# Performance work log

Measured on AMD Instinct MI355X. Metric: run time of the kernel, lower is better.

The kernel has to match this reference:

```python
import jax, jax.numpy as jnp
import numpy as np

B, S, D, H, HD = 1, 4096, 768, 12, 64
L, C, WIN, NCLS = 2, 256, 256, 64
NC = S // C
V, FF = 50265, 3072
NEG = -1e9
SCALE = np.float32(1.0 / np.sqrt(HD))


def setup_inputs() -> dict:
    key = jax.random.key(0)
    ks = jax.random.split(key, 32)
    p = lambda k, shape: (0.02 * jax.random.normal(k, shape)).astype(jnp.float32)
    inp = {
        'x': jax.random.randint(ks[0], (B, S), 0, V, dtype=jnp.int32),
        'mask_src': jnp.ones((B, S), dtype=jnp.int32),
        'clss': jnp.sort(jax.random.randint(ks[1], (B, NCLS), 0, S, dtype=jnp.int32), axis=-1),
        'segs': jax.random.randint(ks[2], (B, S), 0, 2, dtype=jnp.int32),
        'word_emb': p(ks[3], (V, D)),
        'pos_emb': p(ks[4], (S, D)),
        'type_emb': p(ks[5], (2, D)),
        'ln_e_s': jnp.ones((D,), jnp.float32), 'ln_e_b': jnp.zeros((D,), jnp.float32),
        'Wq': p(ks[6], (L, D, D)), 'bq': jnp.zeros((L, D), jnp.float32),
        'Wk': p(ks[7], (L, D, D)), 'bk': jnp.zeros((L, D), jnp.float32),
        'Wv': p(ks[8], (L, D, D)), 'bv': jnp.zeros((L, D), jnp.float32),
        'Wqg': p(ks[9], (L, D, D)), 'bqg': jnp.zeros((L, D), jnp.float32),
        'Wkg': p(ks[10], (L, D, D)), 'bkg': jnp.zeros((L, D), jnp.float32),
        'Wvg': p(ks[11], (L, D, D)), 'bvg': jnp.zeros((L, D), jnp.float32),
        'Wo': p(ks[12], (L, D, D)), 'bo': jnp.zeros((L, D), jnp.float32),
        'ln1_s': jnp.ones((L, D), jnp.float32), 'ln1_b': jnp.zeros((L, D), jnp.float32),
        'Wf1': p(ks[13], (L, D, FF)), 'bf1': jnp.zeros((L, FF), jnp.float32),
        'Wf2': p(ks[14], (L, FF, D)), 'bf2': jnp.zeros((L, D), jnp.float32),
        'ln2_s': jnp.ones((L, D), jnp.float32), 'ln2_b': jnp.zeros((L, D), jnp.float32),
    }
    return inp


def _layer_norm(x, s, b):
    m = jnp.mean(x, -1, keepdims=True)
    v = jnp.mean((x - m) ** 2, -1, keepdims=True)
    return (x - m) * jax.lax.rsqrt(v + 1e-5) * s + b


def _forward(x, mask_src, clss, segs, word_emb, pos_emb, type_emb, ln_e_s, ln_e_b,
             Wq, bq, Wk, bk, Wv, bv, Wqg, bqg, Wkg, bkg, Wvg, bvg, Wo, bo,
             ln1_s, ln1_b, Wf1, bf1, Wf2, bf2, ln2_s, ln2_b):
    # global positions: union of all clss values, same for every batch row
    g_idx = clss.reshape(-1)                                       # [NCLS]
    is_glb = jnp.zeros((S,), bool).at[g_idx].set(True)             # [S]
    kvalid = (mask_src > 0) & (~is_glb)[None, :]                   # band keys: no pad, no global
    gi = (jnp.arange(NC) * C)[:, None] + jnp.arange(3 * C)[None, :]  # gather idx into padded seq
    rel = jnp.arange(3 * C)[None, :] - (jnp.arange(C)[:, None] + C)  # key offset from query
    band_ok = jnp.abs(rel) <= WIN                                   # [C,3C]
    kv3 = jnp.pad(kvalid, ((0, 0), (C, C)))[:, gi]                  # [B,NC,3C]
    bmask = band_ok[None, None, None, :, :] & kv3[:, None, :, None, :]  # [B,1,NC,C,3C]
    gkey_ok = (mask_src[:, g_idx] > 0)[:, None, None, :]            # [B,1,1,NCLS]
    full_ok = (mask_src > 0)[:, None, None, :]                      # [B,1,1,S]

    h = _layer_norm(word_emb[x] + pos_emb[jnp.arange(S)][None] + type_emb[segs], ln_e_s, ln_e_b)

    for l in range(L):
        q = ((h @ Wq[l] + bq[l]).reshape(B, S, H, HD)) * SCALE
        k = (h @ Wk[l] + bk[l]).reshape(B, S, H, HD)
        v = (h @ Wv[l] + bv[l]).reshape(B, S, H, HD)
        # --- sliding-window band attention ---
        k3 = jnp.pad(k, ((0, 0), (C, C), (0, 0), (0, 0)))[:, gi]    # [B,NC,3C,H,HD]
        v3 = jnp.pad(v, ((0, 0), (C, C), (0, 0), (0, 0)))[:, gi]
        qc = q.reshape(B, NC, C, H, HD)
        sb = jnp.einsum('bnqhd,bnkhd->bhnqk', qc, k3)               # [B,H,NC,C,3C]
        sb = jnp.where(bmask, sb, NEG)
        # --- global keys seen by every query ---
        kg, vg = k[:, g_idx], v[:, g_idx]                           # [B,NCLS,H,HD]
        sg = jnp.einsum('bshd,bkhd->bhsk', q, kg)                   # [B,H,S,NCLS]
        sg = jnp.where(gkey_ok, sg, NEG)
        scores = jnp.concatenate([sg, sb.reshape(B, H, S, 3 * C)], -1)
        probs = jax.nn.softmax(scores, axis=-1)
        pg = probs[..., :NCLS]
        pb = probs[..., NCLS:].reshape(B, H, NC, C, 3 * C)
        out = jnp.einsum('bhnqk,bnkhd->bnqhd', pb, v3).reshape(B, S, H, HD)
        out = out + jnp.einsum('bhsk,bkhd->bshd', pg, vg)
        # --- global query tokens: full attention with *_global projections ---
        hg = h[:, g_idx]                                            # [B,NCLS,D]
        qg = ((hg @ Wqg[l] + bqg[l]).reshape(B, NCLS, H, HD)) * SCALE
        kgf = (h @ Wkg[l] + bkg[l]).reshape(B, S, H, HD)
        vgf = (h @ Wvg[l] + bvg[l]).reshape(B, S, H, HD)
        sfull = jnp.einsum('bqhd,bkhd->bhqk', qg, kgf)              # [B,H,NCLS,S]
        sfull = jnp.where(full_ok, sfull, NEG)
        og = jnp.einsum('bhqk,bkhd->bqhd', jax.nn.softmax(sfull, -1), vgf)
        out = out.at[:, g_idx].set(og)
        # --- output proj, residual, LN, FFN ---
        attn_out = out.reshape(B, S, D) @ Wo[l] + bo[l]
        h = _layer_norm(h + attn_out, ln1_s[l], ln1_b[l])
        ff = jax.nn.gelu(h @ Wf1[l] + bf1[l]) @ Wf2[l] + bf2[l]
        h = _layer_norm(h + ff, ln2_s[l], ln2_b[l])
    return h


def reference(x, mask_src, clss, segs, word_emb, pos_emb, type_emb, ln_e_s, ln_e_b,
              Wq, bq, Wk, bk, Wv, bv, Wqg, bqg, Wkg, bkg, Wvg, bvg, Wo, bo,
              ln1_s, ln1_b, Wf1, bf1, Wf2, bf2, ln2_s, ln2_b):
    return _forward(x, mask_src, clss, segs, word_emb, pos_emb, type_emb, ln_e_s, ln_e_b,
                    Wq, bq, Wk, bk, Wv, bv, Wqg, bqg, Wkg, bkg, Wvg, bvg, Wo, bo,
                    ln1_s, ln1_b, Wf1, bf1, Wf2, bf2, ln2_s, ln2_b)
```

## Files before the change

kernel.cpp:

```cpp
#include <hip/hip_runtime.h>
#include <hip/hip_bf16.h>
#include <cstdint>

#define SEQ  4096
#define DIM  768
#define NH   12
#define HDIM 64
#define NLAYER 2
#define CHK  256
#define WINR 256
#define NCLS 64
#define NCHK 16
#define FFD  3072
#define QSCALE 0.125f
#define LOG2E 1.44269504f
#define QSC2 (QSCALE * LOG2E)
#define SD ((size_t)SEQ * DIM)
#define PS_LD 72
#define TK 32

typedef __attribute__((__vector_size__(16))) float floatx4;
typedef __attribute__((ext_vector_type(8))) __bf16 bf16x8;

__device__ __forceinline__ void async16(const void* g, void* l) {
    __builtin_amdgcn_global_load_lds(
        (const __attribute__((address_space(1))) uint32_t*)g,
        (__attribute__((address_space(3))) uint32_t*)l, 16, 0, 0);
}

__device__ __forceinline__ float block_reduce_sum(float v, float* red) {
    int t = threadIdx.x;
    red[t] = v; __syncthreads();
    #pragma unroll
    for (int st = 128; st > 0; st >>= 1) {
        if (t < st) red[t] += red[t + st];
        __syncthreads();
    }
    float r = red[0]; __syncthreads();
    return r;
}

__device__ __forceinline__ float gelu_f(float x) {
    float x3 = x * x * x;
    return 0.5f * x * (1.0f + tanhf(0.7978845608028654f * (x + 0.044715f * x3)));
}

__global__ __launch_bounds__(256) void setup_kernel(
    const float* __restrict__ bq, const float* __restrict__ bk, const float* __restrict__ bv,
    const float* __restrict__ bkg, const float* __restrict__ bvg,
    float* __restrict__ bqkv, int* __restrict__ isglb, int* __restrict__ glb_rank)
{
    int idx = blockIdx.x * 256 + threadIdx.x;
    int l = idx / 3840, c = idx % 3840, j = c / 768, d = c % 768;
    const float* s = (j == 0) ? bq : (j == 1) ? bk : (j == 2) ? bv : (j == 3) ? bkg : bvg;
    bqkv[idx] = s[l * 768 + d];
    if (idx < SEQ) { isglb[idx] = 0; glb_rank[idx] = -1; }
}
__global__ __launch_bounds__(64) void set_rank_kernel(
    const int* __restrict__ clss, int* __restrict__ isglb, int* __restrict__ glb_rank)
{
    int t = threadIdx.x;
    int p = clss[t];
    isglb[p] = 1;
    glb_rank[p] = t;
}

__global__ __launch_bounds__(256) void embed_ln_kernel(
    const int* __restrict__ x, const int* __restrict__ segs,
    const float* __restrict__ word_emb, const float* __restrict__ pos_emb,
    const float* __restrict__ type_emb, const float* __restrict__ gs,
    const float* __restrict__ gb, float* __restrict__ h, __bf16* __restrict__ hb)
{
    __shared__ float red[256];
    int s = blockIdx.x, t = threadIdx.x;
    int w = x[s], sg = segs[s];
    float v0[3]; float lsum = 0.f;
    #pragma unroll
    for (int i = 0; i < 3; i++) {
        int d = t + i * 256;
        float val = word_emb[(size_t)w * DIM + d] + pos_emb[(size_t)s * DIM + d]
                  + type_emb[(size_t)sg * DIM + d];
        v0[i] = val; lsum += val;
    }
    float mean = block_reduce_sum(lsum, red) * (1.0f / DIM);
    float lv = 0.f;
    #pragma unroll
    for (int i = 0; i < 3; i++) { float dv = v0[i] - mean; lv += dv * dv; }
    float var = block_reduce_sum(lv, red) * (1.0f / DIM);
    float rstd = rsqrtf(var + 1e-5f);
    #pragma unroll
    for (int i = 0; i < 3; i++) {
        int d = t + i * 256;
        float o = (v0[i] - mean) * rstd * gs[d] + gb[d];
        h[(size_t)s * DIM + d] = o;
        hb[(size_t)s * DIM + d] = (__bf16)o;
    }
}

__global__ __launch_bounds__(256) void add_ln_kernel(
    float* __restrict__ h, const float* __restrict__ r,
    const float* __restrict__ gs, const float* __restrict__ gb,
    __bf16* __restrict__ hb)
{
    __shared__ float red[256];
    int s = blockIdx.x, t = threadIdx.x;
    float v0[3]; float lsum = 0.f;
    #pragma unroll
    for (int i = 0; i < 3; i++) {
        int d = t + i * 256;
        float val = h[(size_t)s * DIM + d] + r[(size_t)s * DIM + d];
        v0[i] = val; lsum += val;
    }
    float mean = block_reduce_sum(lsum, red) * (1.0f / DIM);
    float lv = 0.f;
    #pragma unroll
    for (int i = 0; i < 3; i++) { float dv = v0[i] - mean; lv += dv * dv; }
    float var = block_reduce_sum(lv, red) * (1.0f / DIM);
    float rstd = rsqrtf(var + 1e-5f);
    #pragma unroll
    for (int i = 0; i < 3; i++) {
        int d = t + i * 256;
        float o = (v0[i] - mean) * rstd * gs[d] + gb[d];
        h[(size_t)s * DIM + d] = o;
        hb[(size_t)s * DIM + d] = (__bf16)o;
    }
}

struct Ptr16 { const float* p[16]; };
__global__ __launch_bounds__(256) void transpose_w_kernel(
    Ptr16 in, __bf16* __restrict__ out, int K, int N)
{
    __shared__ float tile[32][33];
    const float* src = in.p[blockIdx.z];
    __bf16* dst = out + (size_t)blockIdx.z * K * N;
    int bx = blockIdx.x * 32;
    int by = blockIdx.y * 32;
    int tx = threadIdx.x & 31, ty = threadIdx.x >> 5;
    #pragma unroll
    for (int i = 0; i < 32; i += 8)
        tile[ty + i][tx] = src[(size_t)(by + ty + i) * N + bx + tx];
    __syncthreads();
    #pragma unroll
    for (int i = 0; i < 32; i += 8)
        dst[(size_t)(bx + ty + i) * K + by + tx] = (__bf16)tile[tx][ty + i];
}

template<int TMv, int TNv>
__global__ __launch_bounds__(256) void mfma_gemm_t(
    const __bf16* __restrict__ A, const __bf16* __restrict__ Bt,
    const float* __restrict__ bias, float* __restrict__ Cf,
    __bf16* __restrict__ Cb, int M, int N, int K, float scale, int act)
{
    constexpr int AM = TMv / 32, AN = TNv / 32;
    constexpr int CA = TMv / 64, CB = TNv / 64;
    __shared__ __align__(16) __bf16 As[TMv * TK];
    __shared__ __align__(16) __bf16 Bs[TNv * TK];
    int t = threadIdx.x;
    int wave = t >> 6, lane = t & 63;
    int bm = blockIdx.x * TMv, bn = blockIdx.y * TNv;
    int wm = (wave & 1) * (TMv / 2), wn = (wave >> 1) * (TNv / 2);

    floatx4 acc[AM][AN];
    #pragma unroll
    for (int i = 0; i < AM; i++)
        #pragma unroll
        for (int j = 0; j < AN; j++) { floatx4 z = {0.f,0.f,0.f,0.f}; acc[i][j] = z; }

    const int mrow = lane & 15, kq = (lane >> 4) * 8;

    for (int k0 = 0; k0 < K; k0 += TK) {
        __syncthreads();
        #pragma unroll
        for (int i = 0; i < CA; i++) {
            int c = i * 256 + wave * 64 + lane;
            async16(A + (size_t)(bm + (c >> 2)) * K + k0 + (c & 3) * 8,
                    &As[(size_t)(i * 256 + wave * 64) * 8]);
        }
        #pragma unroll
        for (int i = 0; i < CB; i++) {
            int c = i * 256 + wave * 64 + lane;
            async16(Bt + (size_t)(bn + (c >> 2)) * K + k0 + (c & 3) * 8,
                    &Bs[(size_t)(i * 256 + wave * 64) * 8]);
        }
        __builtin_amdgcn_s_waitcnt(0x0f70);
        __syncthreads();
        bf16x8 af[AM], bfr[AN];
        #pragma unroll
        for (int mt = 0; mt < AM; mt++)
            af[mt] = *(const bf16x8*)&As[(wm + mt * 16 + mrow) * TK + kq];
        #pragma unroll
        for (int nt = 0; nt < AN; nt++)
            bfr[nt] = *(const bf16x8*)&Bs[(wn + nt * 16 + mrow) * TK + kq];
        #pragma unroll
        for (int mt = 0; mt < AM; mt++)
            #pragma unroll
            for (int nt = 0; nt < AN; nt++)
                acc[mt][nt] = __builtin_amdgcn_mfma_f32_16x16x32_bf16(
                    af[mt], bfr[nt], acc[mt][nt], 0, 0, 0);
    }

    int col_l = lane & 15, row_l = (lane >> 4) * 4;
    #pragma unroll
    for (int nt = 0; nt < AN; nt++) {
        int col = bn + wn + nt * 16 + col_l;
        float bs = bias[col];
        #pragma unroll
        for (int mt = 0; mt < AM; mt++) {
            floatx4 v = acc[mt][nt];
            int row0 = bm + wm + mt * 16 + row_l;
            #pragma unroll
            for (int rr = 0; rr < 4; rr++) {
                float o = (v[rr] + bs) * scale;
                if (act) o = gelu_f(o);
                if (Cf) Cf[(size_t)(row0 + rr) * N + col] = o;
                if (Cb) Cb[(size_t)(row0 + rr) * N + col] = (__bf16)o;
            }
        }
    }
}

__global__ __launch_bounds__(256) void mfma_gemm_proj(
    const __bf16* __restrict__ A, const __bf16* __restrict__ Bt,
    const float* __restrict__ bias,
    __bf16* __restrict__ qb, __bf16* __restrict__ kb,
    __bf16* __restrict__ vb, __bf16* __restrict__ vtg,
    __bf16* __restrict__ kgb, __bf16* __restrict__ vgt, int K)
{
    __shared__ __align__(16) __bf16 As[128 * TK];
    __shared__ __align__(16) __bf16 Bs[128 * TK];
    int t = threadIdx.x;
    int wave = t >> 6, lane = t & 63;
    int bm = blockIdx.x * 128, bn = blockIdx.y * 128;
    int wm = (wave & 1) * 64, wn = (wave >> 1) * 64;

    floatx4 acc[4][4];
    #pragma unroll
    for (int i = 0; i < 4; i++)
        #pragma unroll
        for (int j = 0; j < 4; j++) { floatx4 z = {0.f,0.f,0.f,0.f}; acc[i][j] = z; }

    const int mrow = lane & 15, kq = (lane >> 4) * 8;

    for (int k0 = 0; k0 < K; k0 += TK) {
        __syncthreads();
        #pragma unroll
        for (int i = 0; i < 2; i++) {
            int c = i * 256 + wave * 64 + lane;
            async16(A + (size_t)(bm + (c >> 2)) * K + k0 + (c & 3) * 8,
                    &As[(size_t)(i * 256 + wave * 64) * 8]);
            async16(Bt + (size_t)(bn + (c >> 2)) * K + k0 + (c & 3) * 8,
                    &Bs[(size_t)(i * 256 + wave * 64) * 8]);
        }
        __builtin_amdgcn_s_waitcnt(0x0f70);
        __syncthreads();
        bf16x8 af[4], bfr[4];
        #pragma unroll
        for (int mt = 0; mt < 4; mt++)
            af[mt] = *(const bf16x8*)&As[(wm + mt * 16 + mrow) * TK + kq];
        #pragma unroll
        for (int nt = 0; nt < 4; nt++)
            bfr[nt] = *(const bf16x8*)&Bs[(wn + nt * 16 + mrow) * TK + kq];
        #pragma unroll
        for (int mt = 0; mt < 4; mt++)
            #pragma unroll
            for (int nt = 0; nt < 4; nt++)
                acc[mt][nt] = __builtin_amdgcn_mfma_f32_16x16x32_bf16(
                    af[mt], bfr[nt], acc[mt][nt], 0, 0, 0);
    }

    int col_l = lane & 15, row_l = (lane >> 4) * 4;
    int seg = bn / 768;
    int colw_base = bn - seg * 768 + wn;
    float scl = (seg == 0) ? QSC2 : 1.0f;
    #pragma unroll
    for (int nt = 0; nt < 4; nt++) {
        int col = bn + wn + nt * 16 + col_l;
        int colw = colw_base + nt * 16 + col_l;
        float bs = bias[col];
        #pragma unroll
        for (int mt = 0; mt < 4; mt++) {
            floatx4 v = acc[mt][nt];
            int row0 = bm + wm + mt * 16 + row_l;
            __bf16 t4[4];
            #pragma unroll
            for (int rr = 0; rr < 4; rr++) t4[rr] = (__bf16)((v[rr] + bs) * scl);
            if (seg <= 2 || seg == 3) {
                __bf16* dst = (seg == 0) ? qb : (seg == 1) ? kb : (seg == 2) ? vb : kgb;
                #pragma unroll
                for (int rr = 0; rr < 4; rr++)
                    dst[(size_t)(row0 + rr) * 768 + colw] = t4[rr];
            }
            if (seg == 2)
                *(uint2*)&vtg[(size_t)colw * SEQ + row0] = *(uint2*)t4;
            if (seg == 4)
                *(uint2*)&vgt[(size_t)colw * SEQ + row0] = *(uint2*)t4;
        }
    }
}

__global__ __launch_bounds__(256) void qg_proj(
    const __bf16* __restrict__ hb, const __bf16* __restrict__ Bt,
    const int* __restrict__ clss, const float* __restrict__ bias,
    __bf16* __restrict__ out)
{
    __shared__ __align__(16) __bf16 As[64 * TK];
    __shared__ __align__(16) __bf16 Bs[128 * TK];
    int t = threadIdx.x;
    int wave = t >> 6, lane = t & 63;
    int bn = blockIdx.y * 128;
    int wm = (wave & 1) * 32, wn = (wave >> 1) * 64;

    int cA = wave * 64 + lane;
    int grow = clss[cA >> 2];

    floatx4 acc[2][4];
    #pragma unroll
    for (int i = 0; i < 2; i++)
        #pragma unroll
        for (int j = 0; j < 4; j++) { floatx4 z = {0.f,0.f,0.f,0.f}; acc[i][j] = z; }

    const int mrow = lane & 15, kq = (lane >> 4) * 8;

    for (int k0 = 0; k0 < DIM; k0 += TK) {
        __syncthreads();
        async16(hb + (size_t)grow * DIM + k0 + (cA & 3) * 8,
                &As[(size_t)(wave * 64) * 8]);
        #pragma unroll
        for (int i = 0; i < 2; i++) {
            int c = i * 256 + wave * 64 + lane;
            async16(Bt + (size_t)(bn + (c >> 2)) * DIM + k0 + (c & 3) * 8,
                    &Bs[(size_t)(i * 256 + wave * 64) * 8]);
        }
        __builtin_amdgcn_s_waitcnt(0x0f70);
        __syncthreads();
        bf16x8 af[2], bfr[4];
        #pragma unroll
        for (int mt = 0; mt < 2; mt++)
            af[mt] = *(const bf16x8*)&As[(wm + mt * 16 + mrow) * TK + kq];
        #pragma unroll
        for (int nt = 0; nt < 4; nt++)
            bfr[nt] = *(const bf16x8*)&Bs[(wn + nt * 16 + mrow) * TK + kq];
        #pragma unroll
        for (int mt = 0; mt < 2; mt++)
            #pragma unroll
            for (int nt = 0; nt < 4; nt++)
                acc[mt][nt] = __builtin_amdgcn_mfma_f32_16x16x32_bf16(
                    af[mt], bfr[nt], acc[mt][nt], 0, 0, 0);
    }
    int col_l = lane & 15, row_l = (lane >> 4) * 4;
    #pragma unroll
    for (int nt = 0; nt < 4; nt++) {
        int col = bn + wn + nt * 16 + col_l;
        float bs = bias[col];
        #pragma unroll
        for (int mt = 0; mt < 2; mt++) {
            floatx4 v = acc[mt][nt];
            int row0 = wm + mt * 16 + row_l;
            #pragma unroll
            for (int rr = 0; rr < 4; rr++)
                out[(size_t)(row0 + rr) * DIM + col] = (__bf16)((v[rr] + bs) * QSC2);
        }
    }
}

__global__ __launch_bounds__(256) void attn_kernel(
    const __bf16* __restrict__ qb, const __bf16* __restrict__ kb,
    const __bf16* __restrict__ vb, const __bf16* __restrict__ vtg,
    const __bf16* __restrict__ qgbb, const __bf16* __restrict__ kgb,
    const __bf16* __restrict__ vgt,
    const int* __restrict__ clss, const int* __restrict__ mask_src,
    const int* __restrict__ is_glb,
    float* __restrict__ OpartB, float* __restrict__ mlpartB,
    float* __restrict__ OpartG, float* __restrict__ mlpartG)
{
    __shared__ __align__(16) __bf16 Kt[4096];
    __shared__ __align__(16) __bf16 Vt[4096];
    __shared__ __align__(16) __bf16 Ps[4][32 * PS_LD];
    __shared__ int kvalid[64];
    __shared__ int gpos[64];

    const int hh = blockIdx.y;
    const int t = threadIdx.x, wave = t >> 6, lane = t & 63;
    const int quad = lane >> 4, col_l = lane & 15, row_l = quad * 4;
    const int l3 = lane & 3, l2h = lane >> 2, l7 = lane & 7, l3h = lane >> 3;
    __bf16* PsW = Ps[wave];

    if (blockIdx.z >= 4) {
        const int sp = blockIdx.x * 2 + (blockIdx.z - 4);
        bf16x8 aq[2];
        {
            const __bf16* qp = qgbb + (size_t)(wave * 16 + col_l) * DIM + hh * HDIM;
            aq[0] = *(const bf16x8*)(qp + quad * 8);
            aq[1] = *(const bf16x8*)(qp + 32 + quad * 8);
        }
        floatx4 oacc[4];
        #pragma unroll
        for (int i = 0; i < 4; i++) { floatx4 z = {0.f,0.f,0.f,0.f}; oacc[i] = z; }
        float m4[4], l4[4];
        #pragma unroll
        for (int r = 0; r < 4; r++) { m4[r] = -1e30f; l4[r] = 0.f; }

        for (int tt = 0; tt < 2; tt++) {
            int pos0 = sp * 128 + tt * 64;
            __syncthreads();
            if (t < 64) kvalid[t] = (mask_src[pos0 + t] > 0) ? 1 : 0;
            #pragma unroll
            for (int ii = 0; ii < 2; ii++) {
                int gid = wave * 2 + ii;
                int p = gid >> 2, kbase = (gid & 3) * 16;
                async16(kgb + (size_t)(pos0 + kbase + l2h) * DIM + hh * HDIM + p * 32 + l3 * 8,
                        &Kt[p * 2048 + kbase * 32]);
            }
            #pragma unroll
            for (int ii = 0; ii < 2; ii++) {
                int gid = wave * 2 + ii;
                int p = gid >> 2, dbase = (gid & 3) * 16;
                async16(vgt + (size_t)(hh * HDIM + dbase + l2h) * SEQ + pos0 + p * 32 + l3 * 8,
                        &Vt[p * 2048 + dbase * 32]);
            }
            __builtin_amdgcn_s_waitcnt(0x0f70);
            __syncthreads();

            floatx4 s[4];
            #pragma unroll
            for (int nt = 0; nt < 4; nt++) {
                bf16x8 b0 = *(const bf16x8*)&Kt[(nt * 16 + col_l) * 32 + quad * 8];
                bf16x8 b1 = *(const bf16x8*)&Kt[2048 + (nt * 16 + col_l) * 32 + quad * 8];
                floatx4 z = {0.f,0.f,0.f,0.f};
                z = __builtin_amdgcn_mfma_f32_16x16x32_bf16(aq[0], b0, z, 0,0,0);
                z = __builtin_amdgcn_mfma_f32_16x16x32_bf16(aq[1], b1, z, 0,0,0);
                s[nt] = z;
            }
            #pragma unroll
            for (int nt = 0; nt < 4; nt++) {
                int kvv = kvalid[nt * 16 + col_l];
                #pragma unroll
                for (int rr = 0; rr < 4; rr++)
                    if (!kvv) s[nt][rr] = -1e30f;
            }
            #pragma unroll
            for (int rr = 0; rr < 4; rr++) {
                float rm = fmaxf(fmaxf(s[0][rr], s[1][rr]), fmaxf(s[2][rr], s[3][rr]));
                rm = fmaxf(rm, __shfl_xor(rm, 1));
                rm = fmaxf(rm, __shfl_xor(rm, 2));
                rm = fmaxf(rm, __shfl_xor(rm, 4));
                rm = fmaxf(rm, __shfl_xor(rm, 8));
                float mo = m4[rr];
                float mn = fmaxf(mo, rm);
                float alpha = exp2f(mo - mn);
                float rsum = 0.f;
                #pragma unroll
                for (int nt = 0; nt < 4; nt++) {
                    float p = exp2f(s[nt][rr] - mn);
                    rsum += p;
                    PsW[(row_l + rr) * PS_LD + nt * 16 + col_l] = (__bf16)p;
                }
                rsum += __shfl_xor(rsum, 1);
                rsum += __shfl_xor(rsum, 2);
                rsum += __shfl_xor(rsum, 4);
                rsum += __shfl_xor(rsum, 8);
                l4[rr] = l4[rr] * alpha + rsum;
                m4[rr] = mn;
                #pragma unroll
                for (int nt = 0; nt < 4; nt++) oacc[nt][rr] *= alpha;
            }
            bf16x8 ap0 = *(const bf16x8*)&PsW[col_l * PS_LD + quad * 8];
            bf16x8 ap1 = *(const bf16x8*)&PsW[col_l * PS_LD + 32 + quad * 8];
            #pragma unroll
            for (int nt = 0; nt < 4; nt++) {
                bf16x8 b0 = *(const bf16x8*)&Vt[(nt * 16 + col_l) * 32 + quad * 8];
                bf16x8 b1 = *(const bf16x8*)&Vt[2048 + (nt * 16 + col_l) * 32 + quad * 8];
                oacc[nt] = __builtin_amdgcn_mfma_f32_16x16x32_bf16(ap0, b0, oacc[nt], 0,0,0);
                oacc[nt] = __builtin_amdgcn_mfma_f32_16x16x32_bf16(ap1, b1, oacc[nt], 0,0,0);
            }
        }
        size_t base = (size_t)(hh * 32 + sp) * 64;
        #pragma unroll
        for (int nt = 0; nt < 4; nt++)
            #pragma unroll
            for (int rr = 0; rr < 4; rr++)
                OpartG[(base + wave * 16 + row_l + rr) * 64 + nt * 16 + col_l] = oacc[nt][rr];
        if (col_l == 0) {
            #pragma unroll
            for (int rr = 0; rr < 4; rr++) {
                mlpartG[(base + wave * 16 + row_l + rr) * 2]     = m4[rr];
                mlpartG[(base + wave * 16 + row_l + rr) * 2 + 1] = l4[rr];
            }
        }
        return;
    }

    const int n = blockIdx.x, zi = blockIdx.z;
    const int qh = zi >> 1, ks = zi & 1;
    const int qw = qh * 128 + wave * 32;

    if (t < 64) gpos[t] = clss[t];

    bf16x8 aq[2][2];
    #pragma unroll
    for (int mt = 0; mt < 2; mt++) {
// ... 118 lines not shown
                float mo = mrw[ri];
                float mn = fmaxf(mo, rm);
                float alpha = exp2f(mo - mn);
                float rsum = 0.f;
                #pragma unroll
                for (int nt = 0; nt < 4; nt++) {
                    float p = exp2f(s[nt][rr] - mn);
                    rsum += p;
                    PsW[(mt * 16 + row_l + rr) * PS_LD + nt * 16 + col_l] = (__bf16)p;
                }
                rsum += __shfl_xor(rsum, 1);
                rsum += __shfl_xor(rsum, 2);
                rsum += __shfl_xor(rsum, 4);
                rsum += __shfl_xor(rsum, 8);
                lrw[ri] = lrw[ri] * alpha + rsum;
                mrw[ri] = mn;
                #pragma unroll
                for (int nt = 0; nt < 4; nt++) oacc[mt][nt][rr] *= alpha;
            }
        }
        bf16x8 bvf[4][2], ap[2][2];
        #pragma unroll
        for (int nt = 0; nt < 4; nt++) {
            bvf[nt][0] = *(const bf16x8*)&Vt[(nt * 16 + col_l) * 32 + quad * 8];
            bvf[nt][1] = *(const bf16x8*)&Vt[2048 + (nt * 16 + col_l) * 32 + quad * 8];
        }
        #pragma unroll
        for (int mt = 0; mt < 2; mt++) {
            ap[mt][0] = *(const bf16x8*)&PsW[(mt * 16 + col_l) * PS_LD + quad * 8];
            ap[mt][1] = *(const bf16x8*)&PsW[(mt * 16 + col_l) * PS_LD + 32 + quad * 8];
        }
        #pragma unroll
        for (int mt = 0; mt < 2; mt++)
            #pragma unroll
            for (int nt = 0; nt < 4; nt++) {
                oacc[mt][nt] = __builtin_amdgcn_mfma_f32_16x16x32_bf16(
                    ap[mt][0], bvf[nt][0], oacc[mt][nt], 0,0,0);
                oacc[mt][nt] = __builtin_amdgcn_mfma_f32_16x16x32_bf16(
                    ap[mt][1], bvf[nt][1], oacc[mt][nt], 0,0,0);
            }
    }

    #pragma unroll
    for (int mt = 0; mt < 2; mt++) {
        #pragma unroll
        for (int rr = 0; rr < 4; rr++) {
            int srow = n * CHK + qw + mt * 16 + row_l + rr;
            size_t rbase = ((size_t)ks * SEQ + srow) * NH + hh;
            #pragma unroll
            for (int nt = 0; nt < 4; nt++)
                OpartB[rbase * 64 + nt * 16 + col_l] = oacc[mt][nt][rr];
            if (col_l == 0) {
                mlpartB[rbase * 2]     = mrw[mt * 4 + rr];
                mlpartB[rbase * 2 + 1] = lrw[mt * 4 + rr];
            }
        }
    }
}

__global__ __launch_bounds__(256) void attn_finalize(
    const float* __restrict__ OpartB, const float* __restrict__ mlpartB,
    const float* __restrict__ OpartG, const float* __restrict__ mlpartG,
    const int* __restrict__ glb_rank, __bf16* __restrict__ outb)
{
    int g = threadIdx.x >> 6, d = threadIdx.x & 63;
    int s = blockIdx.x * 4 + g, hh = blockIdx.y;
    int r = glb_rank[s];
    float o;
    if (r >= 0) {
        float M = -1e30f;
        for (int sp = 0; sp < 32; sp++)
            M = fmaxf(M, mlpartG[(((size_t)hh * 32 + sp) * 64 + r) * 2]);
        float L = 0.f, acc = 0.f;
        for (int sp = 0; sp < 32; sp++) {
            size_t b = ((size_t)hh * 32 + sp) * 64 + r;
            float w = exp2f(mlpartG[b * 2] - M);
            L += mlpartG[b * 2 + 1] * w;
            acc += w * OpartG[b * 64 + d];
        }
        o = acc / L;
    } else {
        size_t r0 = ((size_t)s) * NH + hh;
        size_t r1 = ((size_t)SEQ + s) * NH + hh;
        float m0 = mlpartB[r0 * 2], l0 = mlpartB[r0 * 2 + 1];
        float m1 = mlpartB[r1 * 2], l1 = mlpartB[r1 * 2 + 1];
        float M = fmaxf(m0, m1);
        float w0 = exp2f(m0 - M), w1 = exp2f(m1 - M);
        o = (OpartB[r0 * 64 + d] * w0 + OpartB[r1 * 64 + d] * w1) / (l0 * w0 + l1 * w1);
    }
    outb[(size_t)s * DIM + hh * HDIM + d] = (__bf16)o;
}

extern "C" void kernel_launch(void* const* d_in, const int* in_sizes, int n_in,
                              void* d_out, int out_size, void* d_ws, size_t ws_size,
                              hipStream_t stream)
{
    const int* x        = (const int*)d_in[0];
    const int* mask_src = (const int*)d_in[1];
    const int* clss     = (const int*)d_in[2];
    const int* segs     = (const int*)d_in[3];
    const float* word_emb = (const float*)d_in[4];
    const float* pos_emb  = (const float*)d_in[5];
    const float* type_emb = (const float*)d_in[6];
    const float* ln_e_s   = (const float*)d_in[7];
    const float* ln_e_b   = (const float*)d_in[8];
    const float* Wq  = (const float*)d_in[9];
    const float* bq  = (const float*)d_in[10];
    const float* Wk  = (const float*)d_in[11];
    const float* bk  = (const float*)d_in[12];
    const float* Wv  = (const float*)d_in[13];
    const float* bv  = (const float*)d_in[14];
    const float* Wqg = (const float*)d_in[15];
    const float* bqg = (const float*)d_in[16];
    const float* Wkg = (const float*)d_in[17];
    const float* bkg = (const float*)d_in[18];
    const float* Wvg = (const float*)d_in[19];
    const float* bvg = (const float*)d_in[20];
    const float* Wo  = (const float*)d_in[21];
    const float* bo  = (const float*)d_in[22];
    const float* ln1_s = (const float*)d_in[23];
    const float* ln1_b = (const float*)d_in[24];
    const float* Wf1 = (const float*)d_in[25];
    const float* bf1 = (const float*)d_in[26];
    const float* Wf2 = (const float*)d_in[27];
    const float* bf2 = (const float*)d_in[28];
    const float* ln2_s = (const float*)d_in[29];
    const float* ln2_b = (const float*)d_in[30];

    const size_t DD = (size_t)DIM * DIM;
    float* ws = (float*)d_ws;
    float*  h    = ws;
    float*  s4   = ws + SD;
    __bf16* hb   = (__bf16*)(ws + 2 * SD);
    __bf16* b6b  = (__bf16*)(ws + 2 * SD) + SD;
    __bf16* qb   = (__bf16*)(ws + 3 * SD);
    __bf16* kb   = (__bf16*)(ws + 3 * SD) + SD;
    __bf16* vb   = (__bf16*)(ws + 4 * SD);
    __bf16* vtg  = (__bf16*)(ws + 4 * SD) + SD;
    __bf16* kgb  = (__bf16*)(ws + 5 * SD);
    __bf16* vgt  = (__bf16*)(ws + 5 * SD) + SD;
    __bf16* gelu_b = qb;
    float* extra = ws + 6 * SD;
    __bf16* Wbf   = (__bf16*)extra;
    float* after_w = extra + 15 * DD;
    float* bqkv   = after_w;
    float* OpartG = bqkv + 7680;
    float* mlpartG= OpartG + 1572864;
    float* OpartB = mlpartG + 49152;
    float* mlpartB= OpartB + 6291456;
    __bf16* qgbb  = (__bf16*)(mlpartB + 196608);
    int*   isglb  = (int*)(qgbb + (size_t)NCLS * DIM);
    int*   grank  = isglb + SEQ;

    setup_kernel<<<30, 256, 0, stream>>>(bq, bk, bv, bkg, bvg, bqkv, isglb, grank);
    set_rank_kernel<<<1, 64, 0, stream>>>(clss, isglb, grank);
    embed_ln_kernel<<<SEQ, 256, 0, stream>>>(x, segs, word_emb, pos_emb, type_emb,
                                             ln_e_s, ln_e_b, h, hb);
    {
        Ptr16 wp{};
        wp.p[0] = Wq;        wp.p[1] = Wk;        wp.p[2] = Wv;
        wp.p[3] = Wkg;       wp.p[4] = Wvg;
        wp.p[5] = Wq + DD;   wp.p[6] = Wk + DD;   wp.p[7] = Wv + DD;
        wp.p[8] = Wkg + DD;  wp.p[9] = Wvg + DD;
        wp.p[10] = Wo;       wp.p[11] = Wo + DD;
        wp.p[12] = Wqg;      wp.p[13] = Wqg + DD;
        transpose_w_kernel<<<dim3(24, 24, 14), 256, 0, stream>>>(wp, Wbf, DIM, DIM);
        Ptr16 wf1{};
        wf1.p[0] = Wf1; wf1.p[1] = Wf1 + (size_t)DIM * FFD;
        transpose_w_kernel<<<dim3(96, 24, 2), 256, 0, stream>>>(wf1, Wbf + 14 * DD, DIM, FFD);
        Ptr16 wf2{};
        wf2.p[0] = Wf2; wf2.p[1] = Wf2 + (size_t)FFD * DIM;
        transpose_w_kernel<<<dim3(24, 96, 2), 256, 0, stream>>>(wf2, Wbf + 22 * DD, FFD, DIM);
    }

    for (int l = 0; l < NLAYER; l++) {
        const float* bqg_l = bqg + (size_t)l * DIM;
        const float* bo_l  = bo  + (size_t)l * DIM;
        const float* bf1_l = bf1 + (size_t)l * FFD;
        const float* bf2_l = bf2 + (size_t)l * DIM;

        qg_proj<<<dim3(1, 6), 256, 0, stream>>>(
            hb, Wbf + 12 * DD + (size_t)l * DD, clss, bqg_l, qgbb);
        mfma_gemm_proj<<<dim3(SEQ / 128, 3840 / 128), 256, 0, stream>>>(
            hb, Wbf + (size_t)l * 5 * DD, bqkv + l * 3840,
            qb, kb, vb, vtg, kgb, vgt, DIM);
        attn_kernel<<<dim3(NCHK, NH, 6), 256, 0, stream>>>(
            qb, kb, vb, vtg, qgbb, kgb, vgt, clss, mask_src, isglb,
            OpartB, mlpartB, OpartG, mlpartG);
        attn_finalize<<<dim3(SEQ / 4, NH), 256, 0, stream>>>(
            OpartB, mlpartB, OpartG, mlpartG, grank, b6b);
        mfma_gemm_t<128, 64><<<dim3(SEQ / 128, DIM / 64), 256, 0, stream>>>(
            b6b, Wbf + 10 * DD + (size_t)l * DD, bo_l, s4, nullptr,
            SEQ, DIM, DIM, 1.0f, 0);
        add_ln_kernel<<<SEQ, 256, 0, stream>>>(h, s4, ln1_s + (size_t)l * DIM,
                                               ln1_b + (size_t)l * DIM, hb);
        mfma_gemm_t<128, 128><<<dim3(SEQ / 128, FFD / 128), 256, 0, stream>>>(
            hb, Wbf + 14 * DD + (size_t)l * 4 * DD, bf1_l, nullptr, gelu_b,
            SEQ, FFD, DIM, 1.0f, 1);
        mfma_gemm_t<128, 64><<<dim3(SEQ / 128, DIM / 64), 256, 0, stream>>>(
            gelu_b, Wbf + 22 * DD + (size_t)l * 4 * DD, bf2_l, s4, nullptr,
            SEQ, DIM, FFD, 1.0f, 0);
        add_ln_kernel<<<SEQ, 256, 0, stream>>>(h, s4, ln2_s + (size_t)l * DIM,
                                               ln2_b + (size_t)l * DIM, hb);
    }

    hipMemcpyAsync(d_out, h, SD * sizeof(float), hipMemcpyDeviceToDevice, stream);
}
```

Baseline: 863.6 us.

## Double GEMM K-tile with swizzled LDS, wave-per-row LayerNorm, merge setup kernels

Raises the GEMM K tile from 32 to 64 and stores LDS tiles with an XOR swizzle, so each barrier covers twice the MFMA work and LDS bank conflicts drop. LayerNorm kernels now use one wave per row with float4 loads and shuffle reductions instead of shared-memory tree reductions. Bias packing and all weight transposes are merged into one launch, the setup init moves into the embedding kernel, and the final device copy is removed by writing the last LayerNorm straight to the output. The larger tile doubles LDS use per block, which may lower occupancy.

```diff
diff --git a/kernel.cpp b/kernel.cpp
--- a/kernel.cpp
+++ b/kernel.cpp
@@ -17,10 +17,11 @@
 #define QSC2 (QSCALE * LOG2E)
 #define SD ((size_t)SEQ * DIM)
 #define PS_LD 72
-#define TK 32
+#define TK 64
 
 typedef __attribute__((__vector_size__(16))) float floatx4;
 typedef __attribute__((ext_vector_type(8))) __bf16 bf16x8;
+typedef __attribute__((ext_vector_type(4))) __bf16 bf16x4;
 
 __device__ __forceinline__ void async16(const void* g, void* l) {
     __builtin_amdgcn_global_load_lds(
@@ -28,34 +29,11 @@
         (__attribute__((address_space(3))) uint32_t*)l, 16, 0, 0);
 }
 
-__device__ __forceinline__ float block_reduce_sum(float v, float* red) {
-    int t = threadIdx.x;
-    red[t] = v; __syncthreads();
-    #pragma unroll
-    for (int st = 128; st > 0; st >>= 1) {
-        if (t < st) red[t] += red[t + st];
-        __syncthreads();
-    }
-    float r = red[0]; __syncthreads();
-    return r;
-}
-
 __device__ __forceinline__ float gelu_f(float x) {
     float x3 = x * x * x;
     return 0.5f * x * (1.0f + tanhf(0.7978845608028654f * (x + 0.044715f * x3)));
 }
 
-__global__ __launch_bounds__(256) void setup_kernel(
-    const float* __restrict__ bq, const float* __restrict__ bk, const float* __restrict__ bv,
-    const float* __restrict__ bkg, const float* __restrict__ bvg,
-    float* __restrict__ bqkv, int* __restrict__ isglb, int* __restrict__ glb_rank)
-{
-    int idx = blockIdx.x * 256 + threadIdx.x;
-    int l = idx / 3840, c = idx % 3840, j = c / 768, d = c % 768;
-    const float* s = (j == 0) ? bq : (j == 1) ? bk : (j == 2) ? bv : (j == 3) ? bkg : bvg;
-    bqkv[idx] = s[l * 768 + d];
-    if (idx < SEQ) { isglb[idx] = 0; glb_rank[idx] = -1; }
-}
 __global__ __launch_bounds__(64) void set_rank_kernel(
     const int* __restrict__ clss, int* __restrict__ isglb, int* __restrict__ glb_rank)
 {
@@ -69,72 +47,131 @@
     const int* __restrict__ x, const int* __restrict__ segs,
     const float* __restrict__ word_emb, const float* __restrict__ pos_emb,
     const float* __restrict__ type_emb, const float* __restrict__ gs,
-    const float* __restrict__ gb, float* __restrict__ h, __bf16* __restrict__ hb)
-{
-    __shared__ float red[256];
-    int s = blockIdx.x, t = threadIdx.x;
+    const float* __restrict__ gb, float* __restrict__ h, __bf16* __restrict__ hb,
+    int* __restrict__ isglb, int* __restrict__ grank)
+{
+    int wave = threadIdx.x >> 6, lane = threadIdx.x & 63;
+    int s = blockIdx.x * 4 + wave;
+    if (lane == 0) { isglb[s] = 0; grank[s] = -1; }
     int w = x[s], sg = segs[s];
-    float v0[3]; float lsum = 0.f;
+    const float4* wp = (const float4*)(word_emb + (size_t)w * DIM);
+    const float4* pp = (const float4*)(pos_emb + (size_t)s * DIM);
+    const float4* tp = (const float4*)(type_emb + (size_t)sg * DIM);
+    float4 v[3]; float lsum = 0.f;
     #pragma unroll
     for (int i = 0; i < 3; i++) {
-        int d = t + i * 256;
-        float val = word_emb[(size_t)w * DIM + d] + pos_emb[(size_t)s * DIM + d]
-                  + type_emb[(size_t)sg * DIM + d];
-        v0[i] = val; lsum += val;
-    }
-    float mean = block_reduce_sum(lsum, red) * (1.0f / DIM);
+        int d4 = lane + i * 64;
+        float4 a = wp[d4], b = pp[d4], c = tp[d4];
+        float4 r;
+        r.x = a.x + b.x + c.x; r.y = a.y + b.y + c.y;
+        r.z = a.z + b.z + c.z; r.w = a.w + b.w + c.w;
+        v[i] = r; lsum += r.x + r.y + r.z + r.w;
+    }
+    #pragma unroll
+    for (int st = 32; st > 0; st >>= 1) lsum += __shfl_xor(lsum, st);
+    float mean = lsum * (1.0f / DIM);
     float lv = 0.f;
     #pragma unroll
-    for (int i = 0; i < 3; i++) { float dv = v0[i] - mean; lv += dv * dv; }
-    float var = block_reduce_sum(lv, red) * (1.0f / DIM);
-    float rstd = rsqrtf(var + 1e-5f);
-    #pragma unroll
     for (int i = 0; i < 3; i++) {
-        int d = t + i * 256;
-        float o = (v0[i] - mean) * rstd * gs[d] + gb[d];
-        h[(size_t)s * DIM + d] = o;
-        hb[(size_t)s * DIM + d] = (__bf16)o;
+        float dx = v[i].x - mean, dy = v[i].y - mean, dz = v[i].z - mean, dw = v[i].w - mean;
+        lv += dx * dx + dy * dy + dz * dz + dw * dw;
+    }
+    #pragma unroll
+    for (int st = 32; st > 0; st >>= 1) lv += __shfl_xor(lv, st);
+    float rstd = rsqrtf(lv * (1.0f / DIM) + 1e-5f);
+    #pragma unroll
+    for (int i = 0; i < 3; i++) {
+        int d4 = lane + i * 64;
+        float4 s4v = ((const float4*)gs)[d4], b4v = ((const float4*)gb)[d4];
+        float4 o;
+        o.x = (v[i].x - mean) * rstd * s4v.x + b4v.x;
+        o.y = (v[i].y - mean) * rstd * s4v.y + b4v.y;
+        o.z = (v[i].z - mean) * rstd * s4v.z + b4v.z;
+        o.w = (v[i].w - mean) * rstd * s4v.w + b4v.w;
+        ((float4*)(h + (size_t)s * DIM))[d4] = o;
+        bf16x4 ob; ob[0] = (__bf16)o.x; ob[1] = (__bf16)o.y;
+        ob[2] = (__bf16)o.z; ob[3] = (__bf16)o.w;
+        *(bf16x4*)(hb + (size_t)s * DIM + (size_t)d4 * 4) = ob;
     }
 }
 
 __global__ __launch_bounds__(256) void add_ln_kernel(
-    float* __restrict__ h, const float* __restrict__ r,
+    const float* __restrict__ h, const float* __restrict__ r,
     const float* __restrict__ gs, const float* __restrict__ gb,
-    __bf16* __restrict__ hb)
-{
-    __shared__ float red[256];
-    int s = blockIdx.x, t = threadIdx.x;
-    float v0[3]; float lsum = 0.f;
+    float* __restrict__ hout, __bf16* __restrict__ hb)
+{
+    int wave = threadIdx.x >> 6, lane = threadIdx.x & 63;
+    int s = blockIdx.x * 4 + wave;
+    const float4* hp = (const float4*)(h + (size_t)s * DIM);
+    const float4* rp = (const float4*)(r + (size_t)s * DIM);
+    float4 v[3]; float lsum = 0.f;
     #pragma unroll
     for (int i = 0; i < 3; i++) {
-        int d = t + i * 256;
-        float val = h[(size_t)s * DIM + d] + r[(size_t)s * DIM + d];
-        v0[i] = val; lsum += val;
-    }
-    float mean = block_reduce_sum(lsum, red) * (1.0f / DIM);
+        int d4 = lane + i * 64;
+        float4 a = hp[d4], b = rp[d4];
+        float4 q;
+        q.x = a.x + b.x; q.y = a.y + b.y; q.z = a.z + b.z; q.w = a.w + b.w;
+        v[i] = q; lsum += q.x + q.y + q.z + q.w;
+    }
+    #pragma unroll
+    for (int st = 32; st > 0; st >>= 1) lsum += __shfl_xor(lsum, st);
+    float mean = lsum * (1.0f / DIM);
     float lv = 0.f;
     #pragma unroll
-    for (int i = 0; i < 3; i++) { float dv = v0[i] - mean; lv += dv * dv; }
-    float var = block_reduce_sum(lv, red) * (1.0f / DIM);
-    float rstd = rsqrtf(var + 1e-5f);
-    #pragma unroll
     for (int i = 0; i < 3; i++) {
-        int d = t + i * 256;
-        float o = (v0[i] - mean) * rstd * gs[d] + gb[d];
-        h[(size_t)s * DIM + d] = o;
-        hb[(size_t)s * DIM + d] = (__bf16)o;
-    }
-}
-
-struct Ptr16 { const float* p[16]; };
-__global__ __launch_bounds__(256) void transpose_w_kernel(
-    Ptr16 in, __bf16* __restrict__ out, int K, int N)
-{
+        float dx = v[i].x - mean, dy = v[i].y - mean, dz = v[i].z - mean, dw = v[i].w - mean;
+        lv += dx * dx + dy * dy + dz * dz + dw * dw;
+    }
+    #pragma unroll
+    for (int st = 32; st > 0; st >>= 1) lv += __shfl_xor(lv, st);
+    float rstd = rsqrtf(lv * (1.0f / DIM) + 1e-5f);
+    #pragma unroll
+    for (int i = 0; i < 3; i++) {
+        int d4 = lane + i * 64;
+        float4 s4v = ((const float4*)gs)[d4], b4v = ((const float4*)gb)[d4];
+        float4 o;
+        o.x = (v[i].x - mean) * rstd * s4v.x + b4v.x;
+        o.y = (v[i].y - mean) * rstd * s4v.y + b4v.y;
+        o.z = (v[i].z - mean) * rstd * s4v.z + b4v.z;
+        o.w = (v[i].w - mean) * rstd * s4v.w + b4v.w;
+        ((float4*)(hout + (size_t)s * DIM))[d4] = o;
+        bf16x4 ob; ob[0] = (__bf16)o.x; ob[1] = (__bf16)o.y;
+        ob[2] = (__bf16)o.z; ob[3] = (__bf16)o.w;
+        *(bf16x4*)(hb + (size_t)s * DIM + (size_t)d4 * 4) = ob;
+    }
+}
+
+struct TArgs { const float* p14[14]; const float* f1[2]; const float* f2[2]; };
+#define DD_ ((size_t)DIM * DIM)
+__global__ __launch_bounds__(256) void tpose_setup_kernel(
+    TArgs ta, __bf16* __restrict__ Wbf,
+    const float* __restrict__ bq, const float* __restrict__ bk,
+    const float* __restrict__ bv, const float* __restrict__ bkg,
+    const float* __restrict__ bvg, float* __restrict__ bqkv)
+{
+    int b = blockIdx.x;
+    if (b >= 17280) {
+        int idx = (b - 17280) * 256 + threadIdx.x;
+        int l = idx / 3840, c = idx % 3840, j = c / 768, d = c % 768;
+        const float* s = (j == 0) ? bq : (j == 1) ? bk : (j == 2) ? bv : (j == 3) ? bkg : bvg;
+        bqkv[idx] = s[l * 768 + d];
+        return;
+    }
+    const float* src; __bf16* dst; int K, N, bx, by;
+    if (b < 8064) {
+        int z = b / 576, rr = b % 576;
+        src = ta.p14[z]; dst = Wbf + (size_t)z * DD_;
+        K = 768; N = 768; bx = (rr % 24) * 32; by = (rr / 24) * 32;
+    } else if (b < 12672) {
+        int bb = b - 8064; int z = bb / 2304, rr = bb % 2304;
+        src = ta.f1[z]; dst = Wbf + 14 * DD_ + (size_t)z * 4 * DD_;
+        K = 768; N = 3072; bx = (rr % 96) * 32; by = (rr / 96) * 32;
+    } else {
+        int bb = b - 12672; int z = bb / 2304, rr = bb % 2304;
+        src = ta.f2[z]; dst = Wbf + 22 * DD_ + (size_t)z * 4 * DD_;
+        K = 3072; N = 768; bx = (rr % 24) * 32; by = (rr / 24) * 32;
+    }
     __shared__ float tile[32][33];
-    const float* src = in.p[blockIdx.z];
-    __bf16* dst = out + (size_t)blockIdx.z * K * N;
-    int bx = blockIdx.x * 32;
-    int by = blockIdx.y * 32;
     int tx = threadIdx.x & 31, ty = threadIdx.x >> 5;
     #pragma unroll
     for (int i = 0; i < 32; i += 8)
@@ -152,7 +189,7 @@
     __bf16* __restrict__ Cb, int M, int N, int K, float scale, int act)
 {
     constexpr int AM = TMv / 32, AN = TNv / 32;
-    constexpr int CA = TMv / 64, CB = TNv / 64;
+    constexpr int LA = TMv / 32, LB = TNv / 32;
     __shared__ __align__(16) __bf16 As[TMv * TK];
     __shared__ __align__(16) __bf16 Bs[TNv * TK];
     int t = threadIdx.x;
@@ -167,36 +204,39 @@
         for (int j = 0; j < AN; j++) { floatx4 z = {0.f,0.f,0.f,0.f}; acc[i][j] = z; }
 
     const int mrow = lane & 15, kq = (lane >> 4) * 8;
+    const int tr8 = lane >> 3, c8 = lane & 7;
+    const int scol = (c8 ^ tr8) * 8;
+    const int swz = (lane & 7) << 3;
+    const __bf16* aBase = A  + (size_t)(bm + wave * 8 + tr8) * K + scol;
+    const __bf16* bBase = Bt + (size_t)(bn + wave * 8 + tr8) * K + scol;
 
     for (int k0 = 0; k0 < K; k0 += TK) {
         __syncthreads();
         #pragma unroll
-        for (int i = 0; i < CA; i++) {
-            int c = i * 256 + wave * 64 + lane;
-            async16(A + (size_t)(bm + (c >> 2)) * K + k0 + (c & 3) * 8,
-                    &As[(size_t)(i * 256 + wave * 64) * 8]);
-        }
-        #pragma unroll
-        for (int i = 0; i < CB; i++) {
-            int c = i * 256 + wave * 64 + lane;
-            async16(Bt + (size_t)(bn + (c >> 2)) * K + k0 + (c & 3) * 8,
-                    &Bs[(size_t)(i * 256 + wave * 64) * 8]);
-        }
+        for (int i = 0; i < LA; i++)
+            async16(aBase + k0 + (size_t)i * 32 * K, &As[(size_t)(i * 256 + wave * 64) * 8]);
+        #pragma unroll
+        for (int i = 0; i < LB; i++)
+            async16(bBase + k0 + (size_t)i * 32 * K, &Bs[(size_t)(i * 256 + wave * 64) * 8]);
         __builtin_amdgcn_s_waitcnt(0x0f70);
         __syncthreads();
-        bf16x8 af[AM], bfr[AN];
-        #pragma unroll
-        for (int mt = 0; mt < AM; mt++)
-            af[mt] = *(const bf16x8*)&As[(wm + mt * 16 + mrow) * TK + kq];
-        #pragma unroll
-        for (int nt = 0; nt < AN; nt++)
-            bfr[nt] = *(const bf16x8*)&Bs[(wn + nt * 16 + mrow) * TK + kq];
-        #pragma unroll
-        for (int mt = 0; mt < AM; mt++)
+        #pragma unroll
+        for (int ks = 0; ks < 2; ks++) {
+            const int e = (ks * 32 + kq) ^ swz;
+            bf16x8 af[AM], bfr[AN];
+            #pragma unroll
+            for (int mt = 0; mt < AM; mt++)
+                af[mt] = *(const bf16x8*)&As[(wm + mt * 16 + mrow) * TK + e];
             #pragma unroll
             for (int nt = 0; nt < AN; nt++)
-                acc[mt][nt] = __builtin_amdgcn_mfma_f32_16x16x32_bf16(
-                    af[mt], bfr[nt], acc[mt][nt], 0, 0, 0);
+                bfr[nt] = *(const bf16x8*)&Bs[(wn + nt * 16 + mrow) * TK + e];
+            #pragma unroll
+            for (int mt = 0; mt < AM; mt++)
+                #pragma unroll
+                for (int nt = 0; nt < AN; nt++)
+                    acc[mt][nt] = __builtin_amdgcn_mfma_f32_16x16x32_bf16(
+                        af[mt], bfr[nt], acc[mt][nt], 0, 0, 0);
+        }
     }
 
     int col_l = lane & 15, row_l = (lane >> 4) * 4;
@@ -240,32 +280,38 @@
         for (int j = 0; j < 4; j++) { floatx4 z = {0.f,0.f,0.f,0.f}; acc[i][j] = z; }
 
     const int mrow = lane & 15, kq = (lane >> 4) * 8;
+    const int tr8 = lane >> 3, c8 = lane & 7;
+    const int scol = (c8 ^ tr8) * 8;
+    const int swz = (lane & 7) << 3;
+    const __bf16* aBase = A  + (size_t)(bm + wave * 8 + tr8) * K + scol;
+    const __bf16* bBase = Bt + (size_t)(bn + wave * 8 + tr8) * K + scol;
 
     for (int k0 = 0; k0 < K; k0 += TK) {
         __syncthreads();
         #pragma unroll
-        for (int i = 0; i < 2; i++) {
-            int c = i * 256 + wave * 64 + lane;
-            async16(A + (size_t)(bm + (c >> 2)) * K + k0 + (c & 3) * 8,
-                    &As[(size_t)(i * 256 + wave * 64) * 8]);
-            async16(Bt + (size_t)(bn + (c >> 2)) * K + k0 + (c & 3) * 8,
-                    &Bs[(size_t)(i * 256 + wave * 64) * 8]);
+        for (int i = 0; i < 4; i++) {
+            async16(aBase + k0 + (size_t)i * 32 * K, &As[(size_t)(i * 256 + wave * 64) * 8]);
+            async16(bBase + k0 + (size_t)i * 32 * K, &Bs[(size_t)(i * 256 + wave * 64) * 8]);
         }
         __builtin_amdgcn_s_waitcnt(0x0f70);
         __syncthreads();
-        bf16x8 af[4], bfr[4];
-        #pragma unroll
-        for (int mt = 0; mt < 4; mt++)
-            af[mt] = *(const bf16x8*)&As[(wm + mt * 16 + mrow) * TK + kq];
-        #pragma unroll
-        for (int nt = 0; nt < 4; nt++)
-            bfr[nt] = *(const bf16x8*)&Bs[(wn + nt * 16 + mrow) * TK + kq];
-        #pragma unroll
-        for (int mt = 0; mt < 4; mt++)
+        #pragma unroll
+        for (int ks = 0; ks < 2; ks++) {
+            const int e = (ks * 32 + kq) ^ swz;
+            bf16x8 af[4], bfr[4];
+            #pragma unroll
+            for (int mt = 0; mt < 4; mt++)
+                af[mt] = *(const bf16x8*)&As[(wm + mt * 16 + mrow) * TK + e];
             #pragma unroll
             for (int nt = 0; nt < 4; nt++)
-                acc[mt][nt] = __builtin_amdgcn_mfma_f32_16x16x32_bf16(
-                    af[mt], bfr[nt], acc[mt][nt], 0, 0, 0);
+                bfr[nt] = *(const bf16x8*)&Bs[(wn + nt * 16 + mrow) * TK + e];
+            #pragma unroll
+            for (int mt = 0; mt < 4; mt++)
+                #pragma unroll
+                for (int nt = 0; nt < 4; nt++)
+                    acc[mt][nt] = __builtin_amdgcn_mfma_f32_16x16x32_bf16(
+                        af[mt], bfr[nt], acc[mt][nt], 0, 0, 0);
+        }
     }
 
     int col_l = lane & 15, row_l = (lane >> 4) * 4;
@@ -310,42 +356,48 @@
     int bn = blockIdx.y * 128;
     int wm = (wave & 1) * 32, wn = (wave >> 1) * 64;
 
-    int cA = wave * 64 + lane;
-    int grow = clss[cA >> 2];
+    const int mrow = lane & 15, kq = (lane >> 4) * 8;
+    const int tr8 = lane >> 3, c8 = lane & 7;
+    const int scol = (c8 ^ tr8) * 8;
+    const int swz = (lane & 7) << 3;
+    int arow0 = wave * 8 + tr8;
+    int g0 = clss[arow0], g1 = clss[32 + arow0];
+    const __bf16* a0 = hb + (size_t)g0 * DIM + scol;
+    const __bf16* a1 = hb + (size_t)g1 * DIM + scol;
+    const __bf16* bBase = Bt + (size_t)(bn + wave * 8 + tr8) * DIM + scol;
 
     floatx4 acc[2][4];
     #pragma unroll
     for (int i = 0; i < 2; i++)
         #pragma unroll
         for (int j = 0; j < 4; j++) { floatx4 z = {0.f,0.f,0.f,0.f}; acc[i][j] = z; }
-
-    const int mrow = lane & 15, kq = (lane >> 4) * 8;
 
     for (int k0 = 0; k0 < DIM; k0 += TK) {
         __syncthreads();
-        async16(hb + (size_t)grow * DIM + k0 + (cA & 3) * 8,
-                &As[(size_t)(wave * 64) * 8]);
-        #pragma unroll
-        for (int i = 0; i < 2; i++) {
-            int c = i * 256 + wave * 64 + lane;
-            async16(Bt + (size_t)(bn + (c >> 2)) * DIM + k0 + (c & 3) * 8,
-                    &Bs[(size_t)(i * 256 + wave * 64) * 8]);
-        }
+        async16(a0 + k0, &As[(size_t)(wave * 64) * 8]);
+        async16(a1 + k0, &As[(size_t)(256 + wave * 64) * 8]);
+        #pragma unroll
+        for (int i = 0; i < 4; i++)
+            async16(bBase + k0 + (size_t)i * 32 * DIM, &Bs[(size_t)(i * 256 + wave * 64) * 8]);
         __builtin_amdgcn_s_waitcnt(0x0f70);
         __syncthreads();
-        bf16x8 af[2], bfr[4];
-        #pragma unroll
-        for (int mt = 0; mt < 2; mt++)
-            af[mt] = *(const bf16x8*)&As[(wm + mt * 16 + mrow) * TK + kq];
-        #pragma unroll
-        for (int nt = 0; nt < 4; nt++)
-            bfr[nt] = *(const bf16x8*)&Bs[(wn + nt * 16 + mrow) * TK + kq];
-        #pragma unroll
-        for (int mt = 0; mt < 2; mt++)
+        #pragma unroll
+        for (int ks = 0; ks < 2; ks++) {
+            const int e = (ks * 32 + kq) ^ swz;
+            bf16x8 af[2], bfr[4];
+            #pragma unroll
+            for (int mt = 0; mt < 2; mt++)
+                af[mt] = *(const bf16x8*)&As[(wm + mt * 16 + mrow) * TK + e];
             #pragma unroll
             for (int nt = 0; nt < 4; nt++)
-                acc[mt][nt] = __builtin_amdgcn_mfma_f32_16x16x32_bf16(
-                    af[mt], bfr[nt], acc[mt][nt], 0, 0, 0);
+                bfr[nt] = *(const bf16x8*)&Bs[(wn + nt * 16 + mrow) * TK + e];
+            #pragma unroll
+            for (int mt = 0; mt < 2; mt++)
+                #pragma unroll
+                for (int nt = 0; nt < 4; nt++)
+                    acc[mt][nt] = __builtin_amdgcn_mfma_f32_16x16x32_bf16(
+                        af[mt], bfr[nt], acc[mt][nt], 0, 0, 0);
+        }
     }
     int col_l = lane & 15, row_l = (lane >> 4) * 4;
     #pragma unroll
@@ -770,25 +822,20 @@
     int*   isglb  = (int*)(qgbb + (size_t)NCLS * DIM);
     int*   grank  = isglb + SEQ;
 
-    setup_kernel<<<30, 256, 0, stream>>>(bq, bk, bv, bkg, bvg, bqkv, isglb, grank);
+    embed_ln_kernel<<<SEQ / 4, 256, 0, stream>>>(x, segs, word_emb, pos_emb, type_emb,
+                                                 ln_e_s, ln_e_b, h, hb, isglb, grank);
     set_rank_kernel<<<1, 64, 0, stream>>>(clss, isglb, grank);
-    embed_ln_kernel<<<SEQ, 256, 0, stream>>>(x, segs, word_emb, pos_emb, type_emb,
-                                             ln_e_s, ln_e_b, h, hb);
     {
-        Ptr16 wp{};
-        wp.p[0] = Wq;        wp.p[1] = Wk;        wp.p[2] = Wv;
-        wp.p[3] = Wkg;       wp.p[4] = Wvg;
-        wp.p[5] = Wq + DD;   wp.p[6] = Wk + DD;   wp.p[7] = Wv + DD;
-        wp.p[8] = Wkg + DD;  wp.p[9] = Wvg + DD;
-        wp.p[10] = Wo;       wp.p[11] = Wo + DD;
-        wp.p[12] = Wqg;      wp.p[13] = Wqg + DD;
-        transpose_w_kernel<<<dim3(24, 24, 14), 256, 0, stream>>>(wp, Wbf, DIM, DIM);
-        Ptr16 wf1{};
-        wf1.p[0] = Wf1; wf1.p[1] = Wf1 + (size_t)DIM * FFD;
-        transpose_w_kernel<<<dim3(96, 24, 2), 256, 0, stream>>>(wf1, Wbf + 14 * DD, DIM, FFD);
-        Ptr16 wf2{};
-        wf2.p[0] = Wf2; wf2.p[1] = Wf2 + (size_t)FFD * DIM;
-        transpose_w_kernel<<<dim3(24, 96, 2), 256, 0, stream>>>(wf2, Wbf + 22 * DD, FFD, DIM);
+        TArgs ta{};
+        ta.p14[0] = Wq;        ta.p14[1] = Wk;        ta.p14[2] = Wv;
+        ta.p14[3] = Wkg;       ta.p14[4] = Wvg;
+        ta.p14[5] = Wq + DD;   ta.p14[6] = Wk + DD;   ta.p14[7] = Wv + DD;
+        ta.p14[8] = Wkg + DD;  ta.p14[9] = Wvg + DD;
+        ta.p14[10] = Wo;       ta.p14[11] = Wo + DD;
+        ta.p14[12] = Wqg;      ta.p14[13] = Wqg + DD;
+        ta.f1[0] = Wf1; ta.f1[1] = Wf1 + (size_t)DIM * FFD;
+        ta.f2[0] = Wf2; ta.f2[1] = Wf2 + (size_t)FFD * DIM;
+        tpose_setup_kernel<<<17310, 256, 0, stream>>>(ta, Wbf, bq, bk, bv, bkg, bvg, bqkv);
     }
 
     for (int l = 0; l < NLAYER; l++) {
@@ -810,17 +857,16 @@
         mfma_gemm_t<128, 64><<<dim3(SEQ / 128, DIM / 64), 256, 0, stream>>>(
             b6b, Wbf + 10 * DD + (size_t)l * DD, bo_l, s4, nullptr,
             SEQ, DIM, DIM, 1.0f, 0);
-        add_ln_kernel<<<SEQ, 256, 0, stream>>>(h, s4, ln1_s + (size_t)l * DIM,
-                                               ln1_b + (size_t)l * DIM, hb);
+        add_ln_kernel<<<SEQ / 4, 256, 0, stream>>>(h, s4, ln1_s + (size_t)l * DIM,
+                                                   ln1_b + (size_t)l * DIM, h, hb);
         mfma_gemm_t<128, 128><<<dim3(SEQ / 128, FFD / 128), 256, 0, stream>>>(
             hb, Wbf + 14 * DD + (size_t)l * 4 * DD, bf1_l, nullptr, gelu_b,
             SEQ, FFD, DIM, 1.0f, 1);
         mfma_gemm_t<128, 64><<<dim3(SEQ / 128, DIM / 64), 256, 0, stream>>>(
             gelu_b, Wbf + 22 * DD + (size_t)l * 4 * DD, bf2_l, s4, nullptr,
             SEQ, DIM, FFD, 1.0f, 0);
-        add_ln_kernel<<<SEQ, 256, 0, stream>>>(h, s4, ln2_s + (size_t)l * DIM,
-                                               ln2_b + (size_t)l * DIM, hb);
-    }
-
-    hipMemcpyAsync(d_out, h, SD * sizeof(float), hipMemcpyDeviceToDevice, stream);
-}
+        add_ln_kernel<<<SEQ / 4, 256, 0, stream>>>(h, s4, ln2_s + (size_t)l * DIM,
+                                                   ln2_b + (size_t)l * DIM,
+                                                   (l == NLAYER - 1) ? (float*)d_out : h, hb);
+    }
+}
```

New measurement: 783.9 us. 1.1x faster.
